# Kernel optimization log

Measured on AMD Instinct MI355X. Metric: run time of the kernel, lower is better.

Reference implementation:

```python
import jax, jax.numpy as jnp
import numpy as np

DIM = 1536
HEADS = 12
HD = DIM // HEADS           # 128
C = HD // 2                 # 64 rotary pairs per head
B = 1
F_, H_, W_ = 16, 16, 16
S = F_ * H_ * W_            # 4096
MAXPOS = 1024
EPS = 1e-6
SPLITS = (C - 2 * (C // 3), C // 3, C // 3)  # (22, 21, 21)


def setup_inputs() -> dict:
    key = jax.random.key(0)
    ks = jax.random.split(key, 8)
    std = 0.02
    x = jax.random.normal(ks[0], (B, S, DIM), jnp.float32)
    seq_lens = jnp.full((B,), S, dtype=jnp.int32)
    grid_sizes = jnp.tile(jnp.array([[F_, H_, W_]], jnp.int32), (B, 1))
    # rotary angle table: per split, theta_j = pos / 10000^(j/size)
    angs = []
    pos = jnp.arange(MAXPOS, dtype=jnp.float32)
    for sz in SPLITS:
        inv = 1.0 / (10000.0 ** (jnp.arange(sz, dtype=jnp.float32) / sz))
        angs.append(jnp.outer(pos, inv))
    freqs = jnp.concatenate(angs, axis=1)  # [MAXPOS, C]
    return {
        "x": x,
        "seq_lens": seq_lens,
        "grid_sizes": grid_sizes,
        "freqs": freqs,
        "wq": jax.random.normal(ks[1], (DIM, DIM), jnp.float32) * std,
        "bq": jnp.zeros((DIM,), jnp.float32),
        "wk": jax.random.normal(ks[2], (DIM, DIM), jnp.float32) * std,
        "bk": jnp.zeros((DIM,), jnp.float32),
        "wv": jax.random.normal(ks[3], (DIM, DIM), jnp.float32) * std,
        "bv": jnp.zeros((DIM,), jnp.float32),
        "wo": jax.random.normal(ks[4], (DIM, DIM), jnp.float32) * std,
        "bo": jnp.zeros((DIM,), jnp.float32),
        "gq": jnp.ones((DIM,), jnp.float32),
        "gk": jnp.ones((DIM,), jnp.float32),
    }


def _rms_norm(x, g):
    # x * rsqrt(mean(x^2) + eps) * g  (WanRMSNorm)
    var = jnp.mean(jnp.square(x), axis=-1, keepdims=True)
    return x * jax.lax.rsqrt(var + EPS) * g


def _rope(x, freqs, f, h, w):
    # x: [b, s, n, hd]; freqs: [MAXPOS, C] angles; grid (f,h,w), s = f*h*w
    fa = freqs[:f, : SPLITS[0]]
    ha = freqs[:h, SPLITS[0] : SPLITS[0] + SPLITS[1]]
    wa = freqs[:w, SPLITS[0] + SPLITS[1] :]
    ang = jnp.concatenate(
        [
            jnp.broadcast_to(fa[:, None, None, :], (f, h, w, SPLITS[0])),
            jnp.broadcast_to(ha[None, :, None, :], (f, h, w, SPLITS[1])),
            jnp.broadcast_to(wa[None, None, :, :], (f, h, w, SPLITS[2])),
        ],
        axis=-1,
    ).reshape(f * h * w, 1, C)  # [s, 1, C] broadcasts over heads
    cos, sin = jnp.cos(ang), jnp.sin(ang)
    xr = x[..., 0::2]  # real parts of complex pairs
    xi = x[..., 1::2]  # imag parts
    out_r = xr * cos - xi * sin
    out_i = xr * sin + xi * cos
    return jnp.stack([out_r, out_i], axis=-1).reshape(x.shape)


def reference(x, seq_lens, grid_sizes, freqs, wq, bq, wk, bk, wv, bv, wo, bo, gq, gk):
    b, s = x.shape[:2]
    q = _rms_norm(x @ wq.T + bq, gq).reshape(b, s, HEADS, HD)
    k = _rms_norm(x @ wk.T + bk, gk).reshape(b, s, HEADS, HD)
    v = (x @ wv.T + bv).reshape(b, s, HEADS, HD)
    # all samples share the same grid (static for jit)
    q = _rope(q, freqs, F_, H_, W_)
    k = _rope(k, freqs, F_, H_, W_)
    scale = 1.0 / np.sqrt(HD)
    scores = jnp.einsum("bqnd,bknd->bnqk", q, k) * scale  # [b, n, s, s]
    k_pos = jnp.arange(s)
    mask = k_pos[None, None, None, :] < seq_lens[:, None, None, None]
    scores = scores + jnp.where(mask, 0.0, -1e9)
    attn = jax.nn.softmax(scores, axis=-1)
    out = jnp.einsum("bnqk,bknd->bqnd", attn, v).reshape(b, s, DIM)
    return out @ wo.T + bo
```

## Files before the change

### kernel.cpp

```cpp
#include <hip/hip_runtime.h>
#include <hip/hip_bf16.h>

#define DIM   1536
#define HEADS 12
#define HD    128
#define SEQ   4096
#define QSCALE 0.08838834764831845f
#define LOG2E 1.44269504088896f

typedef __attribute__((ext_vector_type(8))) short short8;
typedef __attribute__((ext_vector_type(4))) float f32x4;
typedef __attribute__((ext_vector_type(16))) float f32x16;

__device__ __forceinline__ unsigned short f2bf(float f) {
    __hip_bfloat16 h = __float2bfloat16(f);
    return *reinterpret_cast<unsigned short*>(&h);
}
__device__ __forceinline__ float bf2f(unsigned short u) {
    return __uint_as_float(((unsigned int)u) << 16);
}
__device__ __forceinline__ void async_cp16(void* lds, const void* g) {
    __builtin_amdgcn_global_load_lds(
        (const __attribute__((address_space(1))) unsigned int*)g,
        (__attribute__((address_space(3))) unsigned int*)lds, 16, 0, 0);
}

__global__ __launch_bounds__(256) void convert_bf16(
    const float* __restrict__ src, __hip_bfloat16* __restrict__ dst, int n8)
{
    const int i = blockIdx.x * 256 + threadIdx.x;
    if (i >= n8) return;
    const float4 a = *reinterpret_cast<const float4*>(src + (size_t)i * 8);
    const float4 b = *reinterpret_cast<const float4*>(src + (size_t)i * 8 + 4);
    uint4 o;
    o.x = (unsigned int)f2bf(a.x) | ((unsigned int)f2bf(a.y) << 16);
    o.y = (unsigned int)f2bf(a.z) | ((unsigned int)f2bf(a.w) << 16);
    o.z = (unsigned int)f2bf(b.x) | ((unsigned int)f2bf(b.y) << 16);
    o.w = (unsigned int)f2bf(b.z) | ((unsigned int)f2bf(b.w) << 16);
    *reinterpret_cast<uint4*>(dst + (size_t)i * 8) = o;
}

__global__ __launch_bounds__(256) void gemm_qkv(
    const __hip_bfloat16* __restrict__ xb,
    const __hip_bfloat16* __restrict__ wqb, const float* __restrict__ bq,
    const __hip_bfloat16* __restrict__ wkb, const float* __restrict__ bk,
    const __hip_bfloat16* __restrict__ wvb, const float* __restrict__ bv,
    __hip_bfloat16* __restrict__ yq, __hip_bfloat16* __restrict__ yk,
    __hip_bfloat16* __restrict__ vrow)
{
    __shared__ __align__(16) short As[128][32];
    __shared__ __align__(16) short Bs[128][32];
    const int z  = blockIdx.z;
    const __hip_bfloat16* W = (z == 0) ? wqb : (z == 1) ? wkb : wvb;
    const float* bias = (z == 0) ? bq : (z == 1) ? bk : bv;
    __hip_bfloat16* outp = (z == 0) ? yq : (z == 1) ? yk : vrow;
    const int bm0 = blockIdx.x * 128;
    const int bn0 = blockIdx.y * 128;
    const int tid  = threadIdx.x;
    const int lane = tid & 63;
    const int wid  = tid >> 6;
    const int wm = (wid >> 1) * 64;
    const int wn = (wid & 1)  * 64;
    const int fr = lane & 15;
    const int fc = (lane >> 4) * 8;
    const int srow = tid >> 2;
    const int scol = (tid & 3) * 8;

    f32x4 acc[4][4] = {};

    for (int kt = 0; kt < DIM; kt += 32) {
        #pragma unroll
        for (int i = 0; i < 2; i++) {
            async_cp16(&As[i * 64 + ((tid >> 6) << 4)][0],
                       xb + (size_t)(bm0 + i * 64 + srow) * DIM + kt + scol);
            async_cp16(&Bs[i * 64 + ((tid >> 6) << 4)][0],
                       W + (size_t)(bn0 + i * 64 + srow) * DIM + kt + scol);
        }
        __syncthreads();
        short8 af[4], bf8[4];
        #pragma unroll
        for (int m = 0; m < 4; m++) af[m]  = *reinterpret_cast<const short8*>(&As[wm + m * 16 + fr][fc]);
        #pragma unroll
        for (int n = 0; n < 4; n++) bf8[n] = *reinterpret_cast<const short8*>(&Bs[wn + n * 16 + fr][fc]);
        #pragma unroll
        for (int m = 0; m < 4; m++)
            #pragma unroll
            for (int n = 0; n < 4; n++)
                acc[m][n] = __builtin_amdgcn_mfma_f32_16x16x32_bf16(af[m], bf8[n], acc[m][n], 0, 0, 0);
        __syncthreads();
    }

    const int crow0 = bm0 + wm + (lane >> 4) * 4;
    const int ccol0 = bn0 + wn + fr;
    #pragma unroll
    for (int n = 0; n < 4; n++) {
        const int col = ccol0 + n * 16;
        const float bb = bias[col];
        #pragma unroll
        for (int m = 0; m < 4; m++)
            #pragma unroll
            for (int r = 0; r < 4; r++)
                outp[(size_t)(crow0 + m * 16 + r) * DIM + col] =
                    __float2bfloat16(acc[m][n][r] + bb);
    }
}

__global__ __launch_bounds__(256) void rmsnorm_rope(
    __hip_bfloat16* __restrict__ yq, __hip_bfloat16* __restrict__ yk,
    const float* __restrict__ gq, const float* __restrict__ gk,
    const float* __restrict__ freqs)
{
    const int s = blockIdx.x;
    const int z = blockIdx.y;
    __hip_bfloat16* y = z ? yk : yq;
    const float* g = z ? gk : gq;
    const int t = threadIdx.x;

    float xr[3], xi[3];
    float ss = 0.f;
    #pragma unroll
    for (int i = 0; i < 3; i++) {
        const int p = t + i * 256;
        const unsigned int uu = *reinterpret_cast<const unsigned int*>(&y[(size_t)s * DIM + 2 * p]);
        xr[i] = bf2f((unsigned short)(uu & 0xffffu));
        xi[i] = bf2f((unsigned short)(uu >> 16));
        ss += xr[i] * xr[i] + xi[i] * xi[i];
    }
    #pragma unroll
    for (int m = 1; m < 64; m <<= 1) ss += __shfl_xor(ss, m, 64);
    __shared__ float red[4];
    if ((t & 63) == 0) red[t >> 6] = ss;
    __syncthreads();
    const float sum = red[0] + red[1] + red[2] + red[3];
    const float rs = rsqrtf(sum * (1.0f / DIM) + 1e-6f);
    const int f = s >> 8, hh = (s >> 4) & 15, ww = s & 15;
    const float osc = z ? 1.0f : QSCALE;
    #pragma unroll
    for (int i = 0; i < 3; i++) {
        const int p = t + i * 256;
        const int cc = p & 63;
        const int pos = (cc < 22) ? f : (cc < 43) ? hh : ww;
        const float ang = freqs[pos * 64 + cc];
        float sn, cs;
        sincosf(ang, &sn, &cs);
        const float a = xr[i] * rs * g[2 * p];
        const float b = xi[i] * rs * g[2 * p + 1];
        const unsigned int pk = (unsigned int)f2bf((a * cs - b * sn) * osc)
                              | ((unsigned int)f2bf((a * sn + b * cs) * osc) << 16);
        *reinterpret_cast<unsigned int*>(&y[(size_t)s * DIM + 2 * p]) = pk;
    }
}

__global__ __launch_bounds__(256) void transpose_v(
    const __hip_bfloat16* __restrict__ vrow,
    __hip_bfloat16* __restrict__ vT)
{
    __shared__ __align__(16) short tile[64][72];
    const int s0 = blockIdx.x * 64;
    const int c0 = blockIdx.y * 64;
    const int t = threadIdx.x;
    #pragma unroll
    for (int i = 0; i < 2; i++) {
        const int ch = t + i * 256;
        const int r = ch >> 3, cc = (ch & 7) * 8;
        *reinterpret_cast<int4*>(&tile[r][cc]) =
            *reinterpret_cast<const int4*>(&vrow[(size_t)(s0 + r) * DIM + c0 + cc]);
    }
    __syncthreads();
    #pragma unroll
    for (int i = 0; i < 2; i++) {
        const int ch = t + i * 256;
        const int c = ch & 63, sc = (ch >> 6) * 8;
        unsigned int w0 = (unsigned short)tile[sc + 0][c] | ((unsigned int)(unsigned short)tile[sc + 1][c] << 16);
        unsigned int w1 = (unsigned short)tile[sc + 2][c] | ((unsigned int)(unsigned short)tile[sc + 3][c] << 16);
        unsigned int w2 = (unsigned short)tile[sc + 4][c] | ((unsigned int)(unsigned short)tile[sc + 5][c] << 16);
        unsigned int w3 = (unsigned short)tile[sc + 6][c] | ((unsigned int)(unsigned short)tile[sc + 7][c] << 16);
        int4 val;
        val.x = (int)w0; val.y = (int)w1; val.z = (int)w2; val.w = (int)w3;
        *reinterpret_cast<int4*>(&vT[(size_t)(c0 + c) * SEQ + s0 + sc]) = val;
    }
}

__global__ __launch_bounds__(256, 2) void flash_attn(
    const __hip_bfloat16* __restrict__ qb,
    const __hip_bfloat16* __restrict__ kb,
    const __hip_bfloat16* __restrict__ vT,
    const int* __restrict__ seq_lens,
    __hip_bfloat16* __restrict__ attno)
{
    __shared__ __align__(16) short Ks[2][64][128];
    __shared__ __align__(16) short Vs[3][128][64];
    const int qt = blockIdx.x;
    const int h  = blockIdx.y;
    const int tid = threadIdx.x;
    const int lane = tid & 63;
    const int w = tid >> 6;
    const int q5 = lane & 31;
    const int hi = lane >> 5;
    const int seqlen = seq_lens[0];
    const int swz = (lane & 7) << 4;
    const int NT = SEQ / 64;

    short8 qf[8];
    const int qrow = qt * 128 + w * 32 + q5;
    #pragma unroll
    for (int s = 0; s < 8; s++)
        qf[s] = *reinterpret_cast<const short8*>(&qb[(size_t)qrow * DIM + h * HD + s * 16 + hi * 8]);

    f32x16 oacc[4] = {};
    float m = -1e30f, l = 0.f;
    unsigned int Wp[2][4][2];

    const int kROW = w * 4 + (lane >> 4);
    const int kCOL = ((lane & 15) ^ (kROW & 7)) * 8;
    const int vROW = w * 8 + (lane >> 3);
    const int vCOL = (((lane & 7) ^ (vROW & 7))) * 8;

    #pragma unroll
    for (int i = 0; i < 4; i++) {
        async_cp16(&Ks[0][i * 16 + w * 4][0],
                   kb + (size_t)(i * 16 + kROW) * DIM + h * HD + kCOL);
        async_cp16(&Vs[0][i * 32 + vROW][0],
                   vT + ((size_t)h * HD + i * 32 + vROW) * SEQ + vCOL);
    }
    __syncthreads();

    {
        #pragma unroll
        for (int i = 0; i < 4; i++) {
            async_cp16(&Ks[1][i * 16 + w * 4][0],
                       kb + (size_t)(64 + i * 16 + kROW) * DIM + h * HD + kCOL);
            async_cp16(&Vs[1][i * 32 + vROW][0],
                       vT + ((size_t)h * HD + i * 32 + vROW) * SEQ + 64 + vCOL);
        }
        const char* Kp = (const char*)&Ks[0][0][0];
        f32x16 sacc[2] = {};
        __builtin_amdgcn_s_setprio(1);
        #pragma unroll
        for (int s = 0; s < 8; s++)
            #pragma unroll
            for (int kbk = 0; kbk < 2; kbk++) {
                short8 kf = *reinterpret_cast<const short8*>(
                    Kp + (kbk * 32 + q5) * 256 + ((s * 32 + hi * 16) ^ swz));
                sacc[kbk] = __builtin_amdgcn_mfma_f32_32x32x16_bf16(kf, qf[s], sacc[kbk], 0, 0, 0);
            }
        __builtin_amdgcn_s_setprio(0);
        float tmax = -1e30f;
        #pragma unroll
        for (int kbk = 0; kbk < 2; kbk++)
            #pragma unroll
            for (int r = 0; r < 16; r++) {
                const int key = kbk * 32 + (r & 3) + 8 * (r >> 2) + 4 * hi;
                const float sv = (key < seqlen) ? sacc[kbk][r] : -1e30f;
                sacc[kbk][r] = sv;
                tmax = fmaxf(tmax, sv);
            }
        tmax = fmaxf(tmax, __shfl_xor(tmax, 32, 64));
        const float mn = fmaxf(m, tmax);
        m = mn;
        float ps = 0.f;
        #pragma unroll
        for (int kbk = 0; kbk < 2; kbk++)
            #pragma unroll
            for (int r = 0; r < 16; r++) {
                const float p = exp2f((sacc[kbk][r] - m) * LOG2E);
                sacc[kbk][r] = p;
                ps += p;
            }
        ps += __shfl_xor(ps, 32, 64);
        l = ps;
        #pragma unroll
        for (int kbk = 0; kbk < 2; kbk++)
            #pragma unroll
            for (int tq = 0; tq < 4; tq++) {
                Wp[kbk][tq][0] = (unsigned int)f2bf(sacc[kbk][4 * tq + 0])
                               | ((unsigned int)f2bf(sacc[kbk][4 * tq + 1]) << 16);
                Wp[kbk][tq][1] = (unsigned int)f2bf(sacc[kbk][4 * tq + 2])
                               | ((unsigned int)f2bf(sacc[kbk][4 * tq + 3]) << 16);
            }
    }

    int vprev = 0, vnext = 2;
    for (int t = 1; t < NT; t++) {
        const int kbase = t * 64;
        __syncthreads();

        if (t + 1 < NT) {
            const int nb = kbase + 64;
            #pragma unroll
            for (int i = 0; i < 4; i++) {
                async_cp16(&Ks[(t + 1) & 1][i * 16 + w * 4][0],
                           kb + (size_t)(nb + i * 16 + kROW) * DIM + h * HD + kCOL);
                async_cp16(&Vs[vnext][i * 32 + vROW][0],
                           vT + ((size_t)h * HD + i * 32 + vROW) * SEQ + nb + vCOL);
            }
        }

        const char* Kp = (const char*)&Ks[t & 1][0][0];
        f32x16 sacc[2] = {};
        __builtin_amdgcn_s_setprio(1);
        #pragma unroll
        for (int s = 0; s < 8; s++)
            #pragma unroll
            for (int kbk = 0; kbk < 2; kbk++) {
                short8 kf = *reinterpret_cast<const short8*>(
                    Kp + (kbk * 32 + q5) * 256 + ((s * 32 + hi * 16) ^ swz));
                sacc[kbk] = __builtin_amdgcn_mfma_f32_32x32x16_bf16(kf, qf[s], sacc[kbk], 0, 0, 0);
            }
        __builtin_amdgcn_s_setprio(0);

        {
            const char* Vp = (const char*)&Vs[vprev][0][0];
            #pragma unroll
            for (int ks = 0; ks < 4; ks++) {
                const int kbk = ks >> 1;
                const int te = (ks & 1) * 2, to = te + 1;
                const int a0 = (int)Wp[kbk][te][0], a1 = (int)Wp[kbk][te][1];
                const int b0 = (int)Wp[kbk][to][0], b1 = (int)Wp[kbk][to][1];
                const int xa0 = __shfl_xor(a0, 32, 64);
                const int xa1 = __shfl_xor(a1, 32, 64);
                const int xb0 = __shfl_xor(b0, 32, 64);
                const int xb1 = __shfl_xor(b1, 32, 64);
                int4 pwv;
                pwv.x = hi ? xb0 : a0;
                pwv.y = hi ? xb1 : a1;
                pwv.z = hi ? b0  : xa0;
                pwv.w = hi ? b1  : xa1;
                const short8 pf = __builtin_bit_cast(short8, pwv);
                __builtin_amdgcn_s_setprio(1);
                #pragma unroll
                for (int cb = 0; cb < 4; cb++) {
                    short8 vf = *reinterpret_cast<const short8*>(
                        Vp + (cb * 32 + q5) * 128 + ((ks * 32 + hi * 16) ^ swz));
                    oacc[cb] = __builtin_amdgcn_mfma_f32_32x32x16_bf16(vf, pf, oacc[cb], 0, 0, 0);
                }
                __builtin_amdgcn_s_setprio(0);
            }
        }

        float tmax = -1e30f;
        if (kbase + 64 <= seqlen) {
            #pragma unroll
            for (int kbk = 0; kbk < 2; kbk++)
                #pragma unroll
                for (int r = 0; r < 16; r++) tmax = fmaxf(tmax, sacc[kbk][r]);
        } else {
            #pragma unroll
            for (int kbk = 0; kbk < 2; kbk++)
                #pragma unroll
                for (int r = 0; r < 16; r++) {
                    const int key = kbase + kbk * 32 + (r & 3) + 8 * (r >> 2) + 4 * hi;
                    const float sv = (key < seqlen) ? sacc[kbk][r] : -1e30f;
                    sacc[kbk][r] = sv;
                    tmax = fmaxf(tmax, sv);
                }
        }
        tmax = fmaxf(tmax, __shfl_xor(tmax, 32, 64));
        if (!__all(tmax <= m + 8.0f)) {
            const float mn = fmaxf(m, tmax);
            const float alpha = exp2f((m - mn) * LOG2E);
            m = mn;
            l *= alpha;
            #pragma unroll
            for (int cb = 0; cb < 4; cb++)
                #pragma unroll
                for (int r = 0; r < 16; r++) oacc[cb][r] *= alpha;
        }
        float ps = 0.f;
        #pragma unroll
        for (int kbk = 0; kbk < 2; kbk++)
            #pragma unroll
            for (int r = 0; r < 16; r++) {
                const float p = exp2f((sacc[kbk][r] - m) * LOG2E);
                sacc[kbk][r] = p;
                ps += p;
            }
        ps += __shfl_xor(ps, 32, 64);
        l += ps;
        #pragma unroll
        for (int kbk = 0; kbk < 2; kbk++)
            #pragma unroll
            for (int tq = 0; tq < 4; tq++) {
                Wp[kbk][tq][0] = (unsigned int)f2bf(sacc[kbk][4 * tq + 0])
                               | ((unsigned int)f2bf(sacc[kbk][4 * tq + 1]) << 16);
                Wp[kbk][tq][1] = (unsigned int)f2bf(sacc[kbk][4 * tq + 2])
                               | ((unsigned int)f2bf(sacc[kbk][4 * tq + 3]) << 16);
            }

        vprev = (vprev == 2) ? 0 : vprev + 1;
        vnext = (vnext == 2) ? 0 : vnext + 1;
    }

    {
        const char* Vp = (const char*)&Vs[vprev][0][0];
        #pragma unroll
        for (int ks = 0; ks < 4; ks++) {
            const int kbk = ks >> 1;
            const int te = (ks & 1) * 2, to = te + 1;
            const int a0 = (int)Wp[kbk][te][0], a1 = (int)Wp[kbk][te][1];
            const int b0 = (int)Wp[kbk][to][0], b1 = (int)Wp[kbk][to][1];
            const int xa0 = __shfl_xor(a0, 32, 64);
            const int xa1 = __shfl_xor(a1, 32, 64);
            const int xb0 = __shfl_xor(b0, 32, 64);
            const int xb1 = __shfl_xor(b1, 32, 64);
            int4 pwv;
            pwv.x = hi ? xb0 : a0;
            pwv.y = hi ? xb1 : a1;
            pwv.z = hi ? b0  : xa0;
            pwv.w = hi ? b1  : xa1;
            const short8 pf = __builtin_bit_cast(short8, pwv);
            #pragma unroll
            for (int cb = 0; cb < 4; cb++) {
                short8 vf = *reinterpret_cast<const short8*>(
                    Vp + (cb * 32 + q5) * 128 + ((ks * 32 + hi * 16) ^ swz));
                oacc[cb] = __builtin_amdgcn_mfma_f32_32x32x16_bf16(vf, pf, oacc[cb], 0, 0, 0);
            }
        }
    }

    const float inv_l = 1.f / l;
    const size_t obase = (size_t)qrow * DIM + h * HD;
    #pragma unroll
    for (int cb = 0; cb < 4; cb++) {
        #pragma unroll
        for (int tq = 0; tq < 4; tq++) {
            uint2 pko;
            pko.x = (unsigned int)f2bf(oacc[cb][4 * tq + 0] * inv_l)
                  | ((unsigned int)f2bf(oacc[cb][4 * tq + 1] * inv_l) << 16);
            pko.y = (unsigned int)f2bf(oacc[cb][4 * tq + 2] * inv_l)
                  | ((unsigned int)f2bf(oacc[cb][4 * tq + 3] * inv_l) << 16);
            *reinterpret_cast<uint2*>(&attno[obase + cb * 32 + 8 * tq + 4 * hi]) = pko;
        }
    }
}

__global__ __launch_bounds__(256) void gemm_out(
    const __hip_bfloat16* __restrict__ A,
    const __hip_bfloat16* __restrict__ W,
    const float* __restrict__ bias,
    float* __restrict__ outp)
{
    __shared__ __align__(16) short As[128][32];
    __shared__ __align__(16) short Bs[128][32];
    const int bm0 = blockIdx.x * 128;
    const int bn0 = blockIdx.y * 128;
    const int tid = threadIdx.x;
    const int lane = tid & 63;
    const int wid = tid >> 6;
    const int wm = (wid >> 1) * 64;
    const int wn = (wid & 1) * 64;
    const int fr = lane & 15;
    const int fc = (lane >> 4) * 8;
    const int srow = tid >> 2;
    const int scol = (tid & 3) * 8;

    f32x4 acc[4][4] = {};

    for (int kt = 0; kt < DIM; kt += 32) {
        #pragma unroll
        for (int i = 0; i < 2; i++) {
            async_cp16(&As[i * 64 + ((tid >> 6) << 4)][0],
                       A + (size_t)(bm0 + i * 64 + srow) * DIM + kt + scol);
            async_cp16(&Bs[i * 64 + ((tid >> 6) << 4)][0],
                       W + (size_t)(bn0 + i * 64 + srow) * DIM + kt + scol);
        }
        __syncthreads();
        short8 af[4], bf8[4];
        #pragma unroll
        for (int m = 0; m < 4; m++) af[m]  = *reinterpret_cast<const short8*>(&As[wm + m * 16 + fr][fc]);
        #pragma unroll
        for (int n = 0; n < 4; n++) bf8[n] = *reinterpret_cast<const short8*>(&Bs[wn + n * 16 + fr][fc]);
        #pragma unroll
        for (int m = 0; m < 4; m++)
            #pragma unroll
            for (int n = 0; n < 4; n++)
                acc[m][n] = __builtin_amdgcn_mfma_f32_16x16x32_bf16(af[m], bf8[n], acc[m][n], 0, 0, 0);
        __syncthreads();
    }

    const int crow0 = bm0 + wm + (lane >> 4) * 4;
    const int ccol0 = bn0 + wn + fr;
    #pragma unroll
    for (int n = 0; n < 4; n++) {
        const int col = ccol0 + n * 16;
        const float bb = bias[col];
        #pragma unroll
        for (int m = 0; m < 4; m++)
            #pragma unroll
            for (int r = 0; r < 4; r++)
                outp[(size_t)(crow0 + m * 16 + r) * DIM + col] = acc[m][n][r] + bb;
    }
}

extern "C" void kernel_launch(void* const* d_in, const int* in_sizes, int n_in,
                              void* d_out, int out_size, void* d_ws, size_t ws_size,
                              hipStream_t stream)
{
    const float* x        = (const float*)d_in[0];
    const int*   seq_lens = (const int*)d_in[1];
    const float* freqs    = (const float*)d_in[3];
    const float* wq = (const float*)d_in[4];
    const float* bq = (const float*)d_in[5];
    const float* wk = (const float*)d_in[6];
    const float* bk = (const float*)d_in[7];
    const float* wv = (const float*)d_in[8];
    const float* bv = (const float*)d_in[9];
    const float* wo = (const float*)d_in[10];
    const float* bo = (const float*)d_in[11];
    const float* gq = (const float*)d_in[12];
    const float* gk = (const float*)d_in[13];
    float* out = (float*)d_out;

    char* ws = (char*)d_ws;
    __hip_bfloat16* yq    = (__hip_bfloat16*)(ws);
    __hip_bfloat16* yk    = (__hip_bfloat16*)(ws + 12582912);
    __hip_bfloat16* vrow  = (__hip_bfloat16*)(ws + 25165824);
    __hip_bfloat16* vT    = (__hip_bfloat16*)(ws + 37748736);
    __hip_bfloat16* attno = (__hip_bfloat16*)(ws + 25165824);
    __hip_bfloat16* xb    = (__hip_bfloat16*)(ws + 37748736);
    __hip_bfloat16* wob   = (__hip_bfloat16*)(ws);
    __hip_bfloat16* wqb   = (__hip_bfloat16*)d_out;
    __hip_bfloat16* wkb   = wqb + 2359296;
    __hip_bfloat16* wvb   = wkb + 2359296;

    dim3 blk(256);
    convert_bf16<<<dim3(3072), blk, 0, stream>>>(x,  xb,  786432);
    convert_bf16<<<dim3(1152), blk, 0, stream>>>(wq, wqb, 294912);
    convert_bf16<<<dim3(1152), blk, 0, stream>>>(wk, wkb, 294912);
    convert_bf16<<<dim3(1152), blk, 0, stream>>>(wv, wvb, 294912);
    gemm_qkv    <<<dim3(32, 12, 3), blk, 0, stream>>>(xb, wqb, bq, wkb, bk, wvb, bv, yq, yk, vrow);
    rmsnorm_rope<<<dim3(4096, 2),   blk, 0, stream>>>(yq, yk, gq, gk, freqs);
    transpose_v <<<dim3(64, 24),    blk, 0, stream>>>(vrow, vT);
    flash_attn  <<<dim3(32, 12),    blk, 0, stream>>>(yq, yk, vT, seq_lens, attno);
    convert_bf16<<<dim3(1152), blk, 0, stream>>>(wo, wob, 294912);
    gemm_out    <<<dim3(32, 12),    blk, 0, stream>>>(attno, wob, bo, out);
}
```

Baseline: 330.1 us.

## Merge input conversions into one launch and split QK MFMA accumulation chains

Replaces the four separate fp32-to-bf16 conversion launches with one combined kernel that picks source and destination by index range, removing three launch overheads and tail effects. In flash attention, the QK^T MFMA chain is split into two independent accumulators that are summed afterwards. This shortens the dependent MFMA chain and, in the loop, lets the PV MFMAs overlap before the sum. The softmax exponent becomes a single fma with a precomputed -m*log2e, and the first tile sets m directly. The extra accumulators use more registers, which may lower occupancy.

```diff
diff --git a/kernel.cpp b/kernel.cpp
--- a/kernel.cpp
+++ b/kernel.cpp
@@ -38,6 +38,30 @@
     o.z = (unsigned int)f2bf(b.x) | ((unsigned int)f2bf(b.y) << 16);
     o.w = (unsigned int)f2bf(b.z) | ((unsigned int)f2bf(b.w) << 16);
     *reinterpret_cast<uint4*>(dst + (size_t)i * 8) = o;
+}
+
+__global__ __launch_bounds__(256) void convert_all(
+    const float* __restrict__ x,  const float* __restrict__ wq,
+    const float* __restrict__ wk, const float* __restrict__ wv,
+    __hip_bfloat16* __restrict__ xb,  __hip_bfloat16* __restrict__ wqb,
+    __hip_bfloat16* __restrict__ wkb, __hip_bfloat16* __restrict__ wvb)
+{
+    const int i = blockIdx.x * 256 + threadIdx.x;
+    const float* src;
+    __hip_bfloat16* dst;
+    int off;
+    if (i < 786432)            { src = x;  dst = xb;  off = i; }
+    else if (i < 1081344)      { src = wq; dst = wqb; off = i - 786432; }
+    else if (i < 1376256)      { src = wk; dst = wkb; off = i - 1081344; }
+    else                       { src = wv; dst = wvb; off = i - 1376256; }
+    const float4 a = *reinterpret_cast<const float4*>(src + (size_t)off * 8);
+    const float4 b = *reinterpret_cast<const float4*>(src + (size_t)off * 8 + 4);
+    uint4 o;
+    o.x = (unsigned int)f2bf(a.x) | ((unsigned int)f2bf(a.y) << 16);
+    o.y = (unsigned int)f2bf(a.z) | ((unsigned int)f2bf(a.w) << 16);
+    o.z = (unsigned int)f2bf(b.x) | ((unsigned int)f2bf(b.y) << 16);
+    o.w = (unsigned int)f2bf(b.z) | ((unsigned int)f2bf(b.w) << 16);
+    *reinterpret_cast<uint4*>(dst + (size_t)off * 8) = o;
 }
 
 __global__ __launch_bounds__(256) void gemm_qkv(
@@ -234,17 +258,27 @@
                        vT + ((size_t)h * HD + i * 32 + vROW) * SEQ + 64 + vCOL);
         }
         const char* Kp = (const char*)&Ks[0][0][0];
-        f32x16 sacc[2] = {};
+        f32x16 sacc[2] = {}, sHi[2] = {};
         __builtin_amdgcn_s_setprio(1);
         #pragma unroll
-        for (int s = 0; s < 8; s++)
+        for (int s = 0; s < 4; s++)
             #pragma unroll
             for (int kbk = 0; kbk < 2; kbk++) {
                 short8 kf = *reinterpret_cast<const short8*>(
                     Kp + (kbk * 32 + q5) * 256 + ((s * 32 + hi * 16) ^ swz));
                 sacc[kbk] = __builtin_amdgcn_mfma_f32_32x32x16_bf16(kf, qf[s], sacc[kbk], 0, 0, 0);
             }
+        #pragma unroll
+        for (int s = 4; s < 8; s++)
+            #pragma unroll
+            for (int kbk = 0; kbk < 2; kbk++) {
+                short8 kf = *reinterpret_cast<const short8*>(
+                    Kp + (kbk * 32 + q5) * 256 + ((s * 32 + hi * 16) ^ swz));
+                sHi[kbk] = __builtin_amdgcn_mfma_f32_32x32x16_bf16(kf, qf[s], sHi[kbk], 0, 0, 0);
+            }
         __builtin_amdgcn_s_setprio(0);
+        sacc[0] += sHi[0];
+        sacc[1] += sHi[1];
         float tmax = -1e30f;
         #pragma unroll
         for (int kbk = 0; kbk < 2; kbk++)
@@ -256,14 +290,14 @@
                 tmax = fmaxf(tmax, sv);
             }
         tmax = fmaxf(tmax, __shfl_xor(tmax, 32, 64));
-        const float mn = fmaxf(m, tmax);
-        m = mn;
+        m = tmax;
+        const float nmL = -m * LOG2E;
         float ps = 0.f;
         #pragma unroll
         for (int kbk = 0; kbk < 2; kbk++)
             #pragma unroll
             for (int r = 0; r < 16; r++) {
-                const float p = exp2f((sacc[kbk][r] - m) * LOG2E);
+                const float p = exp2f(fmaf(sacc[kbk][r], LOG2E, nmL));
                 sacc[kbk][r] = p;
                 ps += p;
             }
@@ -297,15 +331,23 @@
         }
 
         const char* Kp = (const char*)&Ks[t & 1][0][0];
-        f32x16 sacc[2] = {};
+        f32x16 sacc[2] = {}, sHi[2] = {};
         __builtin_amdgcn_s_setprio(1);
         #pragma unroll
-        for (int s = 0; s < 8; s++)
+        for (int s = 0; s < 4; s++)
             #pragma unroll
             for (int kbk = 0; kbk < 2; kbk++) {
                 short8 kf = *reinterpret_cast<const short8*>(
                     Kp + (kbk * 32 + q5) * 256 + ((s * 32 + hi * 16) ^ swz));
                 sacc[kbk] = __builtin_amdgcn_mfma_f32_32x32x16_bf16(kf, qf[s], sacc[kbk], 0, 0, 0);
+            }
+        #pragma unroll
+        for (int s = 4; s < 8; s++)
+            #pragma unroll
+            for (int kbk = 0; kbk < 2; kbk++) {
+                short8 kf = *reinterpret_cast<const short8*>(
+                    Kp + (kbk * 32 + q5) * 256 + ((s * 32 + hi * 16) ^ swz));
+                sHi[kbk] = __builtin_amdgcn_mfma_f32_32x32x16_bf16(kf, qf[s], sHi[kbk], 0, 0, 0);
             }
         __builtin_amdgcn_s_setprio(0);
 
@@ -338,6 +380,8 @@
             }
         }
 
+        sacc[0] += sHi[0];
+        sacc[1] += sHi[1];
         float tmax = -1e30f;
         if (kbase + 64 <= seqlen) {
             #pragma unroll
@@ -366,12 +410,13 @@
                 #pragma unroll
                 for (int r = 0; r < 16; r++) oacc[cb][r] *= alpha;
         }
+        const float nmL = -m * LOG2E;
         float ps = 0.f;
         #pragma unroll
         for (int kbk = 0; kbk < 2; kbk++)
             #pragma unroll
             for (int r = 0; r < 16; r++) {
-                const float p = exp2f((sacc[kbk][r] - m) * LOG2E);
+                const float p = exp2f(fmaf(sacc[kbk][r], LOG2E, nmL));
                 sacc[kbk][r] = p;
                 ps += p;
             }
@@ -524,10 +569,7 @@
     __hip_bfloat16* wvb   = wkb + 2359296;
 
     dim3 blk(256);
-    convert_bf16<<<dim3(3072), blk, 0, stream>>>(x,  xb,  786432);
-    convert_bf16<<<dim3(1152), blk, 0, stream>>>(wq, wqb, 294912);
-    convert_bf16<<<dim3(1152), blk, 0, stream>>>(wk, wkb, 294912);
-    convert_bf16<<<dim3(1152), blk, 0, stream>>>(wv, wvb, 294912);
+    convert_all <<<dim3(6528), blk, 0, stream>>>(x, wq, wk, wv, xb, wqb, wkb, wvb);
     gemm_qkv    <<<dim3(32, 12, 3), blk, 0, stream>>>(xb, wqb, bq, wkb, bk, wvb, bv, yq, yk, vrow);
     rmsnorm_rope<<<dim3(4096, 2),   blk, 0, stream>>>(yq, yk, gq, gk, freqs);
     transpose_v <<<dim3(64, 24),    blk, 0, stream>>>(vrow, vT);
```

After: 328.6 us. Within noise of the previous version (-0.4%).
